# Kernel tuning notes

Hardware: AMD Instinct MI355X
Metric: run time of the kernel (lower is better)

Reference implementation:

```python
import jax, jax.numpy as jnp
from jax import lax
import numpy as np

# Model constants (from init_kwargs)
B, S, H = 1, 2048, 2048
E = 32            # n_routed_experts
G = 4             # n_group
TOPK_GROUP = 2
TOP_K = 4
SCALE = 2.5       # routed_scaling_factor
MOE_I = 1024      # moe_intermediate_size (shared expert: MOE_I * n_shared_experts = 1024)


def setup_inputs() -> dict:
    key = jax.random.key(0)
    ks = jax.random.split(key, 9)
    w_scale = 0.02
    return {
        "hidden_states": jax.random.normal(ks[0], (B, S, H), jnp.float32),
        "gate_weight": jax.random.normal(ks[1], (E, H), jnp.float32) * w_scale,
        "e_score_correction_bias": jnp.zeros((E,), jnp.float32),
        "w1": jax.random.normal(ks[2], (E, MOE_I, H), jnp.float32) * w_scale,
        "w3": jax.random.normal(ks[3], (E, MOE_I, H), jnp.float32) * w_scale,
        "w2": jax.random.normal(ks[4], (E, H, MOE_I), jnp.float32) * w_scale,
        "ws1": jax.random.normal(ks[5], (MOE_I, H), jnp.float32) * w_scale,
        "ws3": jax.random.normal(ks[6], (MOE_I, H), jnp.float32) * w_scale,
        "ws2": jax.random.normal(ks[7], (H, MOE_I), jnp.float32) * w_scale,
    }


def _noaux_tc_gate(x_flat, gate_weight, bias):
    """DeepSeekV3 noaux_tc routing. x_flat: [T,H]. Returns (topk_idx [T,k], topk_w [T,k])."""
    T = x_flat.shape[0]
    logits = x_flat.astype(jnp.float32) @ gate_weight.T            # [T, E]
    scores = jax.nn.sigmoid(logits)                                # [T, E]
    scores_for_choice = scores + bias                              # [T, E]
    # group score = sum of top-2 biased scores within each group
    grp = scores_for_choice.reshape(T, G, E // G)
    group_scores = lax.top_k(grp, 2)[0].sum(-1)                    # [T, G]
    gidx = lax.top_k(group_scores, TOPK_GROUP)[1]                  # [T, topk_group]
    gmask = jax.nn.one_hot(gidx, G, dtype=scores.dtype).sum(1)     # [T, G]
    smask = jnp.repeat(gmask, E // G, axis=1)                      # [T, E]
    masked = jnp.where(smask > 0, scores_for_choice, 0.0)
    topk_idx = lax.top_k(masked, TOP_K)[1]                         # [T, k]
    # weights come from the UNbiased sigmoid scores, renormalized and scaled
    tw = jnp.take_along_axis(scores, topk_idx, axis=1)             # [T, k]
    tw = tw / (tw.sum(-1, keepdims=True) + 1e-20) * SCALE
    return topk_idx, tw


def _swiglu(x, w_gate, w_up, w_down):
    # x: [T,H]; w_gate/w_up: [I,H]; w_down: [H,I]
    return (jax.nn.silu(x @ w_gate.T) * (x @ w_up.T)) @ w_down.T


def reference(hidden_states, gate_weight, e_score_correction_bias, w1, w3, w2, ws1, ws3, ws2):
    b, s, h = hidden_states.shape
    x = hidden_states.reshape(-1, h)                               # [T, H]
    T = x.shape[0]
    topk_idx, topk_w = _noaux_tc_gate(x, gate_weight, e_score_correction_bias)
    # dense combine weights [T, E] (scatter of top-k routing weights)
    combine = jnp.zeros((T, E), x.dtype).at[jnp.arange(T)[:, None], topk_idx].add(topk_w)
    # scan over experts: each expert runs a gated MLP on all tokens, weighted combine
    def body(acc, packed):
        w1e, w3e, w2e, ce = packed                                 # ce: [T]
        return acc + ce[:, None] * _swiglu(x, w1e, w3e, w2e), None
    routed, _ = lax.scan(body, jnp.zeros_like(x), (w1, w3, w2, combine.T))
    shared = _swiglu(x, ws1, ws3, ws2)
    return (routed + shared).reshape(b, s, h)
```

## Files before the change

### kernel.cpp

```cpp
#include <hip/hip_runtime.h>


#define T_TOK 2048
#define HD 2048
#define NE 32
#define NI 1024
#define NG 4
#define GSZ (NE / NG)
#define SCALE_F 2.5f

typedef unsigned short ushort_t;
typedef __attribute__((ext_vector_type(8))) short bf16x8;
typedef __attribute__((ext_vector_type(4))) float f32x4;

__device__ inline ushort_t f2bf(float f) {
  unsigned int x = __float_as_uint(f);
  unsigned int r = (x + 0x7fffu + ((x >> 16) & 1u)) >> 16;
  return (ushort_t)r;
}
__device__ inline unsigned pack2(float a, float b) {
  return (unsigned)f2bf(a) | ((unsigned)f2bf(b) << 16);
}

#define GLDS(gp, lp) \
  __builtin_amdgcn_global_load_lds((const __attribute__((address_space(1))) void*)(gp), \
                                   (__attribute__((address_space(3))) void*)(lp), 16, 0, 0)

#define XB_OFF   0ull
#define CNT_OFF  (XB_OFF + 2ull * T_TOK * HD)
#define OFFS_OFF (CNT_OFF + 256ull)
#define TOK_OFF  (OFFS_OFF + 256ull)
#define BW_OFF   (TOK_OFF + 4ull * NE * T_TOK)
#define SC_OFF   (BW_OFF + 4ull * NE * T_TOK)
#define HR_ROWS  12288
#define HR_OFF   (SC_OFF + 4ull * T_TOK * NE)
#define HS_OFF   (HR_OFF + 2ull * HR_ROWS * NI)

__global__ __launch_bounds__(256) void prep_kernel(const float* __restrict__ x,
    ushort_t* __restrict__ xb, float* __restrict__ out, int* __restrict__ counts) {
  if (blockIdx.x == 0 && threadIdx.x < NE) counts[threadIdx.x] = 0;
  int n4 = T_TOK * HD / 4;
  for (int i = blockIdx.x * blockDim.x + threadIdx.x; i < n4; i += gridDim.x * blockDim.x) {
    float4 v = ((const float4*)x)[i];
    uint2 p;
    p.x = pack2(v.x, v.y);
    p.y = pack2(v.z, v.w);
    ((uint2*)xb)[i] = p;
    ((float4*)out)[i] = make_float4(0.f, 0.f, 0.f, 0.f);
  }
}

__global__ __launch_bounds__(256) void logits_kernel(const float* __restrict__ x,
    const float* __restrict__ gw, float* __restrict__ scores) {
  __shared__ float4 gws[32 * 65];
  __shared__ float4 xs[8 * 64];
  int tid = threadIdx.x;
  int t0 = blockIdx.x * 8;
  const float4* x4 = (const float4*)x;
  const float4* g4 = (const float4*)gw;
  int tok = tid >> 5, e = tid & 31;
  float acc = 0.f;
  for (int c = 0; c < 8; c++) {
    int k4 = c * 64;
    for (int j = tid; j < 32 * 64; j += 256)
      gws[(j >> 6) * 65 + (j & 63)] = g4[(size_t)(j >> 6) * (HD / 4) + k4 + (j & 63)];
    for (int j = tid; j < 8 * 64; j += 256)
      xs[j] = x4[(size_t)(t0 + (j >> 6)) * (HD / 4) + k4 + (j & 63)];
    __syncthreads();
#pragma unroll 8
    for (int c4 = 0; c4 < 64; c4++) {
      float4 xv = xs[tok * 64 + c4];
      float4 wv = gws[e * 65 + c4];
      acc += xv.x * wv.x + xv.y * wv.y + xv.z * wv.z + xv.w * wv.w;
    }
    __syncthreads();
  }
  scores[(size_t)(t0 + tok) * NE + e] = acc;
}

__global__ __launch_bounds__(256) void route_kernel(const float* __restrict__ scores,
    const float* __restrict__ bias, int* __restrict__ counts,
    int* __restrict__ btok, float* __restrict__ bw) {
  int t = blockIdx.x * 256 + threadIdx.x;
  if (t >= T_TOK) return;
  float s[NE], sb[NE];
#pragma unroll
  for (int e = 0; e < NE; e++) {
    float sig = 1.f / (1.f + expf(-scores[(size_t)t * NE + e]));
    s[e] = sig;
    sb[e] = sig + bias[e];
  }
  float gs[NG];
#pragma unroll
  for (int g = 0; g < NG; g++) {
    float m1 = -1e30f, m2 = -1e30f;
#pragma unroll
    for (int j = 0; j < GSZ; j++) {
      float v = sb[g * GSZ + j];
      if (v > m1) { m2 = m1; m1 = v; } else if (v > m2) { m2 = v; }
    }
    gs[g] = m1 + m2;
  }
  int g0 = 0; float bv = -1e30f;
#pragma unroll
  for (int g = 0; g < NG; g++) if (gs[g] > bv) { bv = gs[g]; g0 = g; }
  int g1 = -1; bv = -1e30f;
#pragma unroll
  for (int g = 0; g < NG; g++) if (g != g0 && gs[g] > bv) { bv = gs[g]; g1 = g; }
  unsigned used = 0;
  int idx[4]; float tw[4]; float sum = 0.f;
#pragma unroll
  for (int k = 0; k < 4; k++) {
    float best = -1e30f; int bi = 0;
#pragma unroll
    for (int e = 0; e < NE; e++) {
      int g = e >> 3;
      float v = (g == g0 || g == g1) ? sb[e] : 0.0f;
      if (!((used >> e) & 1u) && v > best) { best = v; bi = e; }
    }
    used |= 1u << bi;
    idx[k] = bi; tw[k] = s[bi]; sum += s[bi];
  }
  float inv = SCALE_F / (sum + 1e-20f);
#pragma unroll
  for (int k = 0; k < 4; k++) {
    int e = idx[k];
    int pos = atomicAdd(&counts[e], 1);
    btok[(size_t)e * T_TOK + pos] = t;
    bw[(size_t)e * T_TOK + pos] = tw[k] * inv;
  }
}

__global__ void offsets_kernel(const int* __restrict__ counts, int* __restrict__ offs) {
  if (blockIdx.x == 0 && threadIdx.x == 0) {
    int o = 0;
    for (int e = 0; e < NE; e++) { offs[e] = o; o += (counts[e] + 127) & ~127; }
    offs[NE] = o;
  }
}

__global__ __launch_bounds__(256) void stage1_kernel(
    const float* __restrict__ w1, const float* __restrict__ w3,
    const float* __restrict__ ws1f, const float* __restrict__ ws3f,
    const ushort_t* __restrict__ xb, const int* __restrict__ counts,
    const int* __restrict__ offs, const int* __restrict__ btok,
    ushort_t* __restrict__ hr, ushort_t* __restrict__ hs) {
  int e = blockIdx.z, mt = blockIdx.y, nt = blockIdx.x;
  int cnt, base;
  const float *W1, *W3;
  ushort_t* ho;
  if (e == NE) {
    cnt = T_TOK; W1 = ws1f; W3 = ws3f; ho = hs; base = 0;
  } else {
    cnt = counts[e];
    if (mt * 128 >= cnt) return;
    W1 = w1 + (size_t)e * NI * HD;
    W3 = w3 + (size_t)e * NI * HD;
    ho = hr; base = offs[e];
  }
  __shared__ __align__(16) ushort_t As[128 * 32];
  __shared__ __align__(16) ushort_t B1s[64 * 40];
  __shared__ __align__(16) ushort_t B3s[64 * 40];
  __shared__ int toks[128];
  int tid = threadIdx.x, wave = tid >> 6, lane = tid & 63;
  if (tid < 128) {
    int m = mt * 128 + tid;
    toks[tid] = (e == NE) ? min(m, T_TOK - 1) : btok[(size_t)e * T_TOK + min(m, cnt - 1)];
  }
  __syncthreads();
  int lm = lane & 15, lq = lane >> 4;
  int nbase = nt * 64;
  int ar = wave * 16 + (lane >> 2);
  int acol = (lane & 3) * 8;
  const ushort_t* ag0 = xb + (size_t)toks[ar] * HD + acol;
  const ushort_t* ag1 = xb + (size_t)toks[64 + ar] * HD + acol;
  ushort_t* al0 = As + wave * 512 + lane * 8;
  ushort_t* al1 = As + 2048 + wave * 512 + lane * 8;
  int br = tid >> 2, bc = (tid & 3) * 8;
  const float* b1g = W1 + (size_t)(nbase + br) * HD + bc;
  const float* b3g = W3 + (size_t)(nbase + br) * HD + bc;
  ushort_t* b1l = B1s + br * 40 + bc;
  ushort_t* b3l = B3s + br * 40 + bc;

  f32x4 acc1[2][4], acc3[2][4];
#pragma unroll
  for (int i = 0; i < 2; i++)
#pragma unroll
    for (int j = 0; j < 4; j++) {
      acc1[i][j] = (f32x4){0.f, 0.f, 0.f, 0.f};
      acc3[i][j] = (f32x4){0.f, 0.f, 0.f, 0.f};
    }

  for (int kb = 0; kb < HD / 32; kb++) {
    int k0 = kb * 32;
    GLDS(ag0 + k0, al0);
    GLDS(ag1 + k0, al1);
    {
      float4 v0 = *(const float4*)(b1g + k0);
      float4 v1 = *(const float4*)(b1g + k0 + 4);
      uint4 p;
      p.x = pack2(v0.x, v0.y); p.y = pack2(v0.z, v0.w);
      p.z = pack2(v1.x, v1.y); p.w = pack2(v1.z, v1.w);
      *(uint4*)b1l = p;
    }
    {
      float4 v0 = *(const float4*)(b3g + k0);
      float4 v1 = *(const float4*)(b3g + k0 + 4);
      uint4 p;
      p.x = pack2(v0.x, v0.y); p.y = pack2(v0.z, v0.w);
      p.z = pack2(v1.x, v1.y); p.w = pack2(v1.z, v1.w);
      *(uint4*)b3l = p;
    }
    __syncthreads();
    bf16x8 a0 = *(const bf16x8*)(As + (wave * 32 + lm) * 32 + lq * 8);
    bf16x8 a1 = *(const bf16x8*)(As + (wave * 32 + 16 + lm) * 32 + lq * 8);
#pragma unroll
    for (int n4 = 0; n4 < 4; n4++) {
      bf16x8 b1 = *(const bf16x8*)(B1s + (n4 * 16 + lm) * 40 + lq * 8);
      bf16x8 b3 = *(const bf16x8*)(B3s + (n4 * 16 + lm) * 40 + lq * 8);
      acc1[0][n4] = __builtin_amdgcn_mfma_f32_16x16x32_bf16(a0, b1, acc1[0][n4], 0, 0, 0);
      acc1[1][n4] = __builtin_amdgcn_mfma_f32_16x16x32_bf16(a1, b1, acc1[1][n4], 0, 0, 0);
      acc3[0][n4] = __builtin_amdgcn_mfma_f32_16x16x32_bf16(a0, b3, acc3[0][n4], 0, 0, 0);
      acc3[1][n4] = __builtin_amdgcn_mfma_f32_16x16x32_bf16(a1, b3, acc3[1][n4], 0, 0, 0);
    }
    __syncthreads();
  }
#pragma unroll
  for (int i = 0; i < 2; i++)
#pragma unroll
    for (int n4 = 0; n4 < 4; n4++)
#pragma unroll
      for (int r = 0; r < 4; r++) {
        int row = wave * 32 + i * 16 + lq * 4 + r;
        float g = acc1[i][n4][r], u = acc3[i][n4][r];
        float hv = (g / (1.f + __expf(-g))) * u;
        ho[(size_t)(base + mt * 128 + row) * NI + nbase + n4 * 16 + lm] = f2bf(hv);
      }
}

__global__ __launch_bounds__(256) void stage2_kernel(
    const float* __restrict__ w2, const float* __restrict__ ws2f,
    const ushort_t* __restrict__ hr, const ushort_t* __restrict__ hs,
    const int* __restrict__ counts, const int* __restrict__ offs,
    const int* __restrict__ btok, const float* __restrict__ bw,
    float* __restrict__ out) {
  int e = blockIdx.z, mt = blockIdx.y, nt = blockIdx.x;
  int cnt, base;
  const float* W2;
  const ushort_t* hsrc;
  if (e == NE) {
    cnt = T_TOK; W2 = ws2f; hsrc = hs; base = 0;
  } else {
    cnt = counts[e];
    if (mt * 128 >= cnt) return;
    W2 = w2 + (size_t)e * HD * NI;
    hsrc = hr; base = offs[e];
  }
  __shared__ __align__(16) ushort_t As[128 * 32];
  __shared__ __align__(16) ushort_t Bs[128 * 40];
  __shared__ int toks[128];
  __shared__ float wts[128];
  int tid = threadIdx.x, wave = tid >> 6, lane = tid & 63;
  if (tid < 128) {
    int m = mt * 128 + tid;
    if (e == NE) { toks[tid] = m; wts[tid] = 1.f; }
    else {
      int mm = min(m, cnt - 1);
      toks[tid] = btok[(size_t)e * T_TOK + mm];
      wts[tid] = bw[(size_t)e * T_TOK + mm];
    }
  }
  __syncthreads();
  int lm = lane & 15, lq = lane >> 4;
  int wr = wave >> 1, wc = wave & 1;
  const ushort_t* ag = hsrc + (size_t)(base + mt * 128) * NI;
  int ar = wave * 16 + (lane >> 2);
  int acol = (lane & 3) * 8;
  const ushort_t* ag0 = ag + (size_t)ar * NI + acol;
  const ushort_t* ag1 = ag + (size_t)(64 + ar) * NI + acol;
  ushort_t* al0 = As + wave * 512 + lane * 8;
  ushort_t* al1 = As + 2048 + wave * 512 + lane * 8;
  int br = tid >> 2, bc = (tid & 3) * 8;
  const float* bg0 = W2 + (size_t)(nt * 128 + br) * NI + bc;
  const float* bg1 = W2 + (size_t)(nt * 128 + 64 + br) * NI + bc;
  ushort_t* bl0 = Bs + br * 40 + bc;
  ushort_t* bl1 = Bs + (64 + br) * 40 + bc;

  f32x4 acc[4][4];
#pragma unroll
  for (int i = 0; i < 4; i++)
#pragma unroll
    for (int j = 0; j < 4; j++) acc[i][j] = (f32x4){0.f, 0.f, 0.f, 0.f};

  for (int kb = 0; kb < NI / 32; kb++) {
    int k0 = kb * 32;
    GLDS(ag0 + k0, al0);
    GLDS(ag1 + k0, al1);
    {
      float4 v0 = *(const float4*)(bg0 + k0);
      float4 v1 = *(const float4*)(bg0 + k0 + 4);
      uint4 p;
      p.x = pack2(v0.x, v0.y); p.y = pack2(v0.z, v0.w);
      p.z = pack2(v1.x, v1.y); p.w = pack2(v1.z, v1.w);
      *(uint4*)bl0 = p;
    }
    {
      float4 v0 = *(const float4*)(bg1 + k0);
      float4 v1 = *(const float4*)(bg1 + k0 + 4);
      uint4 p;
      p.x = pack2(v0.x, v0.y); p.y = pack2(v0.z, v0.w);
      p.z = pack2(v1.x, v1.y); p.w = pack2(v1.z, v1.w);
      *(uint4*)bl1 = p;
    }
    __syncthreads();
    bf16x8 a[4], b[4];
#pragma unroll
    for (int i = 0; i < 4; i++)
      a[i] = *(const bf16x8*)(As + (wr * 64 + i * 16 + lm) * 32 + lq * 8);
#pragma unroll
    for (int j = 0; j < 4; j++)
      b[j] = *(const bf16x8*)(Bs + (wc * 64 + j * 16 + lm) * 40 + lq * 8);
#pragma unroll
    for (int i = 0; i < 4; i++)
#pragma unroll
      for (int j = 0; j < 4; j++)
        acc[i][j] = __builtin_amdgcn_mfma_f32_16x16x32_bf16(a[i], b[j], acc[i][j], 0, 0, 0);
    __syncthreads();
  }
#pragma unroll
  for (int i = 0; i < 4; i++)
#pragma unroll
    for (int j = 0; j < 4; j++)
#pragma unroll
      for (int r = 0; r < 4; r++) {
        int m = wr * 64 + i * 16 + lq * 4 + r;
        if (mt * 128 + m < cnt) {
          float v = acc[i][j][r] * wts[m];
          atomicAdd(out + (size_t)toks[m] * HD + nt * 128 + wc * 64 + j * 16 + lm, v);
        }
      }
}

extern "C" void kernel_launch(void* const* d_in, const int* in_sizes, int n_in,
                              void* d_out, int out_size, void* d_ws, size_t ws_size,
                              hipStream_t stream) {
  const float* x    = (const float*)d_in[0];
  const float* gw   = (const float*)d_in[1];
  const float* bias = (const float*)d_in[2];
  const float* w1   = (const float*)d_in[3];
  const float* w3   = (const float*)d_in[4];
  const float* w2   = (const float*)d_in[5];
  const float* ws1  = (const float*)d_in[6];
  const float* ws3  = (const float*)d_in[7];
  const float* ws2  = (const float*)d_in[8];
  float* out = (float*)d_out;
  char* ws = (char*)d_ws;

  ushort_t* xb  = (ushort_t*)(ws + XB_OFF);
  int* counts   = (int*)(ws + CNT_OFF);
  int* offs     = (int*)(ws + OFFS_OFF);
  int* btok     = (int*)(ws + TOK_OFF);
  float* bwts   = (float*)(ws + BW_OFF);
  float* scores = (float*)(ws + SC_OFF);
  ushort_t* hr  = (ushort_t*)(ws + HR_OFF);
  ushort_t* hs  = (ushort_t*)(ws + HS_OFF);

  prep_kernel<<<1024, 256, 0, stream>>>(x, xb, out, counts);
  logits_kernel<<<T_TOK / 8, 256, 0, stream>>>(x, gw, scores);
  route_kernel<<<T_TOK / 256, 256, 0, stream>>>(scores, bias, counts, btok, bwts);
  offsets_kernel<<<1, 64, 0, stream>>>(counts, offs);
  stage1_kernel<<<dim3(NI / 64, T_TOK / 128, NE + 1), 256, 0, stream>>>(
      w1, w3, ws1, ws3, xb, counts, offs, btok, hr, hs);
  stage2_kernel<<<dim3(HD / 128, T_TOK / 128, NE + 1), 256, 0, stream>>>(
      w2, ws2, hr, hs, counts, offs, btok, bwts, out);
}
```

Measured before the change: 1.009 ms.

## Double K-tile to 64 with XOR-swizzled LDS, hardware bf16 pack, parallel offsets scan

Both MoE GEMM stages now stage a 64-wide K slice per iteration instead of 32, which halves the number of barrier pairs and loop iterations. The activation tile in LDS uses an XOR swizzle on 16-byte chunks to avoid bank conflicts on the MFMA fragment reads. Software bf16 rounding is replaced by the v_cvt_pk_bf16_f32 instruction, and the offsets kernel becomes a wave-level shuffle scan. LDS use per block roughly doubles, which may lower occupancy.

```diff
diff --git a/kernel.cpp b/kernel.cpp
--- a/kernel.cpp
+++ b/kernel.cpp
@@ -13,14 +13,12 @@
 typedef __attribute__((ext_vector_type(8))) short bf16x8;
 typedef __attribute__((ext_vector_type(4))) float f32x4;
 
-__device__ inline ushort_t f2bf(float f) {
-  unsigned int x = __float_as_uint(f);
-  unsigned int r = (x + 0x7fffu + ((x >> 16) & 1u)) >> 16;
-  return (ushort_t)r;
-}
-__device__ inline unsigned pack2(float a, float b) {
-  return (unsigned)f2bf(a) | ((unsigned)f2bf(b) << 16);
-}
+__device__ inline unsigned cvtpk2(float a, float b) {
+  unsigned r;
+  asm("v_cvt_pk_bf16_f32 %0, %1, %2" : "=v"(r) : "v"(a), "v"(b));
+  return r;
+}
+__device__ inline ushort_t f2bf1(float f) { return (ushort_t)(cvtpk2(f, f) & 0xffffu); }
 
 #define GLDS(gp, lp) \
   __builtin_amdgcn_global_load_lds((const __attribute__((address_space(1))) void*)(gp), \
@@ -43,8 +41,8 @@
   for (int i = blockIdx.x * blockDim.x + threadIdx.x; i < n4; i += gridDim.x * blockDim.x) {
     float4 v = ((const float4*)x)[i];
     uint2 p;
-    p.x = pack2(v.x, v.y);
-    p.y = pack2(v.z, v.w);
+    p.x = cvtpk2(v.x, v.y);
+    p.y = cvtpk2(v.z, v.w);
     ((uint2*)xb)[i] = p;
     ((float4*)out)[i] = make_float4(0.f, 0.f, 0.f, 0.f);
   }
@@ -132,11 +130,15 @@
 }
 
 __global__ void offsets_kernel(const int* __restrict__ counts, int* __restrict__ offs) {
-  if (blockIdx.x == 0 && threadIdx.x == 0) {
-    int o = 0;
-    for (int e = 0; e < NE; e++) { offs[e] = o; o += (counts[e] + 127) & ~127; }
-    offs[NE] = o;
-  }
+  int lane = threadIdx.x;
+  int s = (lane < NE) ? ((counts[lane] + 127) & ~127) : 0;
+#pragma unroll
+  for (int d = 1; d < 64; d <<= 1) {
+    int n = __shfl_up(s, d);
+    if (lane >= d) s += n;
+  }
+  if (lane == 0) offs[0] = 0;
+  if (lane < NE) offs[lane + 1] = s;
 }
 
 __global__ __launch_bounds__(256) void stage1_kernel(
@@ -158,9 +160,9 @@
     W3 = w3 + (size_t)e * NI * HD;
     ho = hr; base = offs[e];
   }
-  __shared__ __align__(16) ushort_t As[128 * 32];
-  __shared__ __align__(16) ushort_t B1s[64 * 40];
-  __shared__ __align__(16) ushort_t B3s[64 * 40];
+  __shared__ __align__(16) ushort_t As[128 * 64];
+  __shared__ __align__(16) ushort_t B1s[64 * 72];
+  __shared__ __align__(16) ushort_t B3s[64 * 72];
   __shared__ int toks[128];
   int tid = threadIdx.x, wave = tid >> 6, lane = tid & 63;
   if (tid < 128) {
@@ -170,17 +172,20 @@
   __syncthreads();
   int lm = lane & 15, lq = lane >> 4;
   int nbase = nt * 64;
-  int ar = wave * 16 + (lane >> 2);
-  int acol = (lane & 3) * 8;
-  const ushort_t* ag0 = xb + (size_t)toks[ar] * HD + acol;
-  const ushort_t* ag1 = xb + (size_t)toks[64 + ar] * HD + acol;
-  ushort_t* al0 = As + wave * 512 + lane * 8;
-  ushort_t* al1 = As + 2048 + wave * 512 + lane * 8;
-  int br = tid >> 2, bc = (tid & 3) * 8;
+  int swz = ((lane & 7) ^ ((lane >> 3) & 7)) * 8;
+  const ushort_t* ag[4];
+  ushort_t* al[4];
+#pragma unroll
+  for (int i = 0; i < 4; i++) {
+    int r = i * 32 + wave * 8 + (lane >> 3);
+    ag[i] = xb + (size_t)toks[r] * HD + swz;
+    al[i] = As + i * 2048 + wave * 512 + lane * 8;
+  }
+  int br = tid >> 2, bc = (tid & 3) * 16;
   const float* b1g = W1 + (size_t)(nbase + br) * HD + bc;
   const float* b3g = W3 + (size_t)(nbase + br) * HD + bc;
-  ushort_t* b1l = B1s + br * 40 + bc;
-  ushort_t* b3l = B3s + br * 40 + bc;
+  ushort_t* b1l = B1s + br * 72 + bc;
+  ushort_t* b3l = B3s + br * 72 + bc;
 
   f32x4 acc1[2][4], acc3[2][4];
 #pragma unroll
@@ -191,37 +196,51 @@
       acc3[i][j] = (f32x4){0.f, 0.f, 0.f, 0.f};
     }
 
-  for (int kb = 0; kb < HD / 32; kb++) {
-    int k0 = kb * 32;
-    GLDS(ag0 + k0, al0);
-    GLDS(ag1 + k0, al1);
+  for (int kb = 0; kb < HD / 64; kb++) {
+    int k0 = kb * 64;
+#pragma unroll
+    for (int i = 0; i < 4; i++) GLDS(ag[i] + k0, al[i]);
     {
       float4 v0 = *(const float4*)(b1g + k0);
       float4 v1 = *(const float4*)(b1g + k0 + 4);
-      uint4 p;
-      p.x = pack2(v0.x, v0.y); p.y = pack2(v0.z, v0.w);
-      p.z = pack2(v1.x, v1.y); p.w = pack2(v1.z, v1.w);
-      *(uint4*)b1l = p;
+      float4 v2 = *(const float4*)(b1g + k0 + 8);
+      float4 v3 = *(const float4*)(b1g + k0 + 12);
+      uint4 p0, p1;
+      p0.x = cvtpk2(v0.x, v0.y); p0.y = cvtpk2(v0.z, v0.w);
+      p0.z = cvtpk2(v1.x, v1.y); p0.w = cvtpk2(v1.z, v1.w);
+      p1.x = cvtpk2(v2.x, v2.y); p1.y = cvtpk2(v2.z, v2.w);
+      p1.z = cvtpk2(v3.x, v3.y); p1.w = cvtpk2(v3.z, v3.w);
+      *(uint4*)b1l = p0;
+      *(uint4*)(b1l + 8) = p1;
     }
     {
       float4 v0 = *(const float4*)(b3g + k0);
       float4 v1 = *(const float4*)(b3g + k0 + 4);
-      uint4 p;
-      p.x = pack2(v0.x, v0.y); p.y = pack2(v0.z, v0.w);
-      p.z = pack2(v1.x, v1.y); p.w = pack2(v1.z, v1.w);
-      *(uint4*)b3l = p;
-    }
-    __syncthreads();
-    bf16x8 a0 = *(const bf16x8*)(As + (wave * 32 + lm) * 32 + lq * 8);
-    bf16x8 a1 = *(const bf16x8*)(As + (wave * 32 + 16 + lm) * 32 + lq * 8);
-#pragma unroll
-    for (int n4 = 0; n4 < 4; n4++) {
-      bf16x8 b1 = *(const bf16x8*)(B1s + (n4 * 16 + lm) * 40 + lq * 8);
-      bf16x8 b3 = *(const bf16x8*)(B3s + (n4 * 16 + lm) * 40 + lq * 8);
-      acc1[0][n4] = __builtin_amdgcn_mfma_f32_16x16x32_bf16(a0, b1, acc1[0][n4], 0, 0, 0);
-      acc1[1][n4] = __builtin_amdgcn_mfma_f32_16x16x32_bf16(a1, b1, acc1[1][n4], 0, 0, 0);
-      acc3[0][n4] = __builtin_amdgcn_mfma_f32_16x16x32_bf16(a0, b3, acc3[0][n4], 0, 0, 0);
-      acc3[1][n4] = __builtin_amdgcn_mfma_f32_16x16x32_bf16(a1, b3, acc3[1][n4], 0, 0, 0);
+      float4 v2 = *(const float4*)(b3g + k0 + 8);
+      float4 v3 = *(const float4*)(b3g + k0 + 12);
+      uint4 p0, p1;
+      p0.x = cvtpk2(v0.x, v0.y); p0.y = cvtpk2(v0.z, v0.w);
+      p0.z = cvtpk2(v1.x, v1.y); p0.w = cvtpk2(v1.z, v1.w);
+      p1.x = cvtpk2(v2.x, v2.y); p1.y = cvtpk2(v2.z, v2.w);
+      p1.z = cvtpk2(v3.x, v3.y); p1.w = cvtpk2(v3.z, v3.w);
+      *(uint4*)b3l = p0;
+      *(uint4*)(b3l + 8) = p1;
+    }
+    __syncthreads();
+#pragma unroll
+    for (int ks = 0; ks < 2; ks++) {
+      int ach = ((ks * 4 + lq) ^ (lm & 7)) * 8;
+      bf16x8 a0 = *(const bf16x8*)(As + (wave * 32 + lm) * 64 + ach);
+      bf16x8 a1 = *(const bf16x8*)(As + (wave * 32 + 16 + lm) * 64 + ach);
+#pragma unroll
+      for (int n4 = 0; n4 < 4; n4++) {
+        bf16x8 b1 = *(const bf16x8*)(B1s + (n4 * 16 + lm) * 72 + ks * 32 + lq * 8);
+        bf16x8 b3 = *(const bf16x8*)(B3s + (n4 * 16 + lm) * 72 + ks * 32 + lq * 8);
+        acc1[0][n4] = __builtin_amdgcn_mfma_f32_16x16x32_bf16(a0, b1, acc1[0][n4], 0, 0, 0);
+        acc1[1][n4] = __builtin_amdgcn_mfma_f32_16x16x32_bf16(a1, b1, acc1[1][n4], 0, 0, 0);
+        acc3[0][n4] = __builtin_amdgcn_mfma_f32_16x16x32_bf16(a0, b3, acc3[0][n4], 0, 0, 0);
+        acc3[1][n4] = __builtin_amdgcn_mfma_f32_16x16x32_bf16(a1, b3, acc3[1][n4], 0, 0, 0);
+      }
     }
     __syncthreads();
   }
@@ -234,7 +253,7 @@
         int row = wave * 32 + i * 16 + lq * 4 + r;
         float g = acc1[i][n4][r], u = acc3[i][n4][r];
         float hv = (g / (1.f + __expf(-g))) * u;
-        ho[(size_t)(base + mt * 128 + row) * NI + nbase + n4 * 16 + lm] = f2bf(hv);
+        ho[(size_t)(base + mt * 128 + row) * NI + nbase + n4 * 16 + lm] = f2bf1(hv);
       }
 }
 
@@ -256,8 +275,8 @@
     W2 = w2 + (size_t)e * HD * NI;
     hsrc = hr; base = offs[e];
   }
-  __shared__ __align__(16) ushort_t As[128 * 32];
-  __shared__ __align__(16) ushort_t Bs[128 * 40];
+  __shared__ __align__(16) ushort_t As[128 * 64];
+  __shared__ __align__(16) ushort_t Bs[128 * 72];
   __shared__ int toks[128];
   __shared__ float wts[128];
   int tid = threadIdx.x, wave = tid >> 6, lane = tid & 63;
@@ -273,18 +292,21 @@
   __syncthreads();
   int lm = lane & 15, lq = lane >> 4;
   int wr = wave >> 1, wc = wave & 1;
-  const ushort_t* ag = hsrc + (size_t)(base + mt * 128) * NI;
-  int ar = wave * 16 + (lane >> 2);
-  int acol = (lane & 3) * 8;
-  const ushort_t* ag0 = ag + (size_t)ar * NI + acol;
-  const ushort_t* ag1 = ag + (size_t)(64 + ar) * NI + acol;
-  ushort_t* al0 = As + wave * 512 + lane * 8;
-  ushort_t* al1 = As + 2048 + wave * 512 + lane * 8;
-  int br = tid >> 2, bc = (tid & 3) * 8;
+  int swz = ((lane & 7) ^ ((lane >> 3) & 7)) * 8;
+  const ushort_t* agbase = hsrc + (size_t)(base + mt * 128) * NI;
+  const ushort_t* ag[4];
+  ushort_t* al[4];
+#pragma unroll
+  for (int i = 0; i < 4; i++) {
+    int r = i * 32 + wave * 8 + (lane >> 3);
+    ag[i] = agbase + (size_t)r * NI + swz;
+    al[i] = As + i * 2048 + wave * 512 + lane * 8;
+  }
+  int br = tid >> 2, bc = (tid & 3) * 16;
   const float* bg0 = W2 + (size_t)(nt * 128 + br) * NI + bc;
   const float* bg1 = W2 + (size_t)(nt * 128 + 64 + br) * NI + bc;
-  ushort_t* bl0 = Bs + br * 40 + bc;
-  ushort_t* bl1 = Bs + (64 + br) * 40 + bc;
+  ushort_t* bl0 = Bs + br * 72 + bc;
+  ushort_t* bl1 = Bs + (64 + br) * 72 + bc;
 
   f32x4 acc[4][4];
 #pragma unroll
@@ -292,39 +314,53 @@
 #pragma unroll
     for (int j = 0; j < 4; j++) acc[i][j] = (f32x4){0.f, 0.f, 0.f, 0.f};
 
-  for (int kb = 0; kb < NI / 32; kb++) {
-    int k0 = kb * 32;
-    GLDS(ag0 + k0, al0);
-    GLDS(ag1 + k0, al1);
+  for (int kb = 0; kb < NI / 64; kb++) {
+    int k0 = kb * 64;
+#pragma unroll
+    for (int i = 0; i < 4; i++) GLDS(ag[i] + k0, al[i]);
     {
       float4 v0 = *(const float4*)(bg0 + k0);
       float4 v1 = *(const float4*)(bg0 + k0 + 4);
-      uint4 p;
-      p.x = pack2(v0.x, v0.y); p.y = pack2(v0.z, v0.w);
-      p.z = pack2(v1.x, v1.y); p.w = pack2(v1.z, v1.w);
-      *(uint4*)bl0 = p;
+      float4 v2 = *(const float4*)(bg0 + k0 + 8);
+      float4 v3 = *(const float4*)(bg0 + k0 + 12);
+      uint4 p0, p1;
+      p0.x = cvtpk2(v0.x, v0.y); p0.y = cvtpk2(v0.z, v0.w);
+      p0.z = cvtpk2(v1.x, v1.y); p0.w = cvtpk2(v1.z, v1.w);
+      p1.x = cvtpk2(v2.x, v2.y); p1.y = cvtpk2(v2.z, v2.w);
+      p1.z = cvtpk2(v3.x, v3.y); p1.w = cvtpk2(v3.z, v3.w);
+      *(uint4*)bl0 = p0;
+      *(uint4*)(bl0 + 8) = p1;
     }
     {
       float4 v0 = *(const float4*)(bg1 + k0);
       float4 v1 = *(const float4*)(bg1 + k0 + 4);
-      uint4 p;
-      p.x = pack2(v0.x, v0.y); p.y = pack2(v0.z, v0.w);
-      p.z = pack2(v1.x, v1.y); p.w = pack2(v1.z, v1.w);
-      *(uint4*)bl1 = p;
-    }
-    __syncthreads();
-    bf16x8 a[4], b[4];
-#pragma unroll
-    for (int i = 0; i < 4; i++)
-      a[i] = *(const bf16x8*)(As + (wr * 64 + i * 16 + lm) * 32 + lq * 8);
-#pragma unroll
-    for (int j = 0; j < 4; j++)
-      b[j] = *(const bf16x8*)(Bs + (wc * 64 + j * 16 + lm) * 40 + lq * 8);
-#pragma unroll
-    for (int i = 0; i < 4; i++)
+      float4 v2 = *(const float4*)(bg1 + k0 + 8);
+      float4 v3 = *(const float4*)(bg1 + k0 + 12);
+      uint4 p0, p1;
+      p0.x = cvtpk2(v0.x, v0.y); p0.y = cvtpk2(v0.z, v0.w);
+      p0.z = cvtpk2(v1.x, v1.y); p0.w = cvtpk2(v1.z, v1.w);
+      p1.x = cvtpk2(v2.x, v2.y); p1.y = cvtpk2(v2.z, v2.w);
+      p1.z = cvtpk2(v3.x, v3.y); p1.w = cvtpk2(v3.z, v3.w);
+      *(uint4*)bl1 = p0;
+      *(uint4*)(bl1 + 8) = p1;
+    }
+    __syncthreads();
+#pragma unroll
+    for (int ks = 0; ks < 2; ks++) {
+      int ach = ((ks * 4 + lq) ^ (lm & 7)) * 8;
+      bf16x8 a[4], b[4];
+#pragma unroll
+      for (int i = 0; i < 4; i++)
+        a[i] = *(const bf16x8*)(As + (wr * 64 + i * 16 + lm) * 64 + ach);
 #pragma unroll
       for (int j = 0; j < 4; j++)
-        acc[i][j] = __builtin_amdgcn_mfma_f32_16x16x32_bf16(a[i], b[j], acc[i][j], 0, 0, 0);
+        b[j] = *(const bf16x8*)(Bs + (wc * 64 + j * 16 + lm) * 72 + ks * 32 + lq * 8);
+#pragma unroll
+      for (int i = 0; i < 4; i++)
+#pragma unroll
+        for (int j = 0; j < 4; j++)
+          acc[i][j] = __builtin_amdgcn_mfma_f32_16x16x32_bf16(a[i], b[j], acc[i][j], 0, 0, 0);
+    }
     __syncthreads();
   }
 #pragma unroll
```

New measurement: 965.9 us. 1.04x faster.
